# Kernel optimization log

Measured on AMD Instinct MI355X. Metric: run time of the kernel, lower is better.

Reference implementation:

```python
import jax, jax.numpy as jnp
import numpy as np
from jax.scipy import special

B, N, DIM, H, DK, DV, F = 2, 1536, 1536, 8, 64, 64, 192


def _pos_embed(seq_len, feat):
    """Enformer relative positional basis: [2*seq_len-1, feat]."""
    per = feat // 6  # 3 basis families x (symmetric, antisymmetric)
    d = jnp.arange(-seq_len + 1, seq_len, dtype=jnp.float32)
    ad = jnp.abs(d)[:, None]  # [2N-1, 1]
    # exponential decay, log-spaced half lives
    half_life = 2.0 ** jnp.linspace(3.0, float(np.log2(seq_len)), per)
    expo = jnp.exp(-jnp.log(2.0) / half_life * ad)
    # central binary mask
    widths = 2.0 ** jnp.arange(1, per + 1, dtype=jnp.float32) - 1.0
    cmask = (widths > ad).astype(jnp.float32)
    # gamma pdf basis
    stddev = seq_len / (2.0 * per)
    start_mean = seq_len / per
    mean = jnp.linspace(start_mean, float(seq_len), per)
    conc = (mean / stddev) ** 2
    rate = mean / stddev ** 2
    log_unnorm = special.xlogy(conc - 1.0, ad) - rate * ad
    log_norm = special.gammaln(conc) - conc * jnp.log(rate)
    probs = jnp.exp(log_unnorm - log_norm) + 1e-8
    gamma = probs / jnp.max(probs, axis=-1, keepdims=True)
    emb = jnp.concatenate([expo, cmask, gamma], axis=-1)
    emb = jnp.concatenate([emb, jnp.sign(d)[:, None] * emb], axis=-1)
    return emb.astype(jnp.float32)


def _relative_shift(x):
    # x: [B, H, N, 2N-1] -> [B, H, N, N] (Transformer-XL shift)
    b, h, t1, t2 = x.shape
    x = jnp.pad(x, ((0, 0), (0, 0), (0, 0), (1, 0)))  # [B,H,N,2N]
    x = x.reshape(b, h, t2 + 1, t1)[:, :, 1:, :].reshape(b, h, t1, t2)
    return x[..., : (t2 + 2) // 2]


def setup_inputs() -> dict:
    key = jax.random.key(0)
    ks = jax.random.split(key, 8)
    s = 0.02
    return {
        "x": jax.random.normal(ks[0], (B, N, DIM), dtype=jnp.float32),
        "Wq": jax.random.normal(ks[1], (DIM, H * DK), dtype=jnp.float32) * s,
        "Wk": jax.random.normal(ks[2], (DIM, H * DK), dtype=jnp.float32) * s,
        "Wv": jax.random.normal(ks[3], (DIM, H * DV), dtype=jnp.float32) * s,
        "Wrel": jax.random.normal(ks[4], (F, H * DK), dtype=jnp.float32) * s,
        "Wout": jax.random.normal(ks[5], (H * DV, DIM), dtype=jnp.float32) * s,
        "bout": jnp.zeros((DIM,), dtype=jnp.float32),
        "rel_content_bias": jax.random.normal(ks[6], (1, H, 1, DK), dtype=jnp.float32),
        "rel_pos_bias": jax.random.normal(ks[7], (1, H, 1, DK), dtype=jnp.float32),
        "pos_embed": _pos_embed(N, F),  # [2N-1, F] buffer
    }


def reference(x, Wq, Wk, Wv, Wrel, Wout, bout, rel_content_bias, rel_pos_bias, pos_embed):
    b, n, _ = x.shape
    h, dk = rel_content_bias.shape[1], rel_content_bias.shape[3]
    dv = Wv.shape[1] // h
    scale = dk ** -0.5
    q = (x @ Wq).reshape(b, n, h, dk).transpose(0, 2, 1, 3) * scale  # [b,h,n,dk]
    k = (x @ Wk).reshape(b, n, h, dk).transpose(0, 2, 1, 3)
    v = (x @ Wv).reshape(b, n, h, dv).transpose(0, 2, 1, 3)
    content_logits = jnp.einsum('bhid,bhjd->bhij', q + rel_content_bias, k)
    rel_k = (pos_embed @ Wrel).reshape(-1, h, dk).transpose(1, 0, 2)  # [h,2n-1,dk]
    rel_logits = jnp.einsum('bhid,hjd->bhij', q + rel_pos_bias, rel_k)  # [b,h,n,2n-1]
    rel_logits = _relative_shift(rel_logits)  # [b,h,n,n]
    attn = jax.nn.softmax(content_logits + rel_logits, axis=-1)
    out = jnp.einsum('bhij,bhjd->bhid', attn, v)
    out = out.transpose(0, 2, 1, 3).reshape(b, n, h * dv)
    return out @ Wout + bout
```

## Files before the change

### kernel.cpp

```cpp
#include <hip/hip_runtime.h>

#define NSEQ  1536
#define HEADS 8
#define NREL  3071
#define NRELP 3072

typedef __bf16 bf16;
typedef __bf16 bf16x8 __attribute__((ext_vector_type(8)));
typedef __bf16 bf16x4 __attribute__((ext_vector_type(4)));
typedef float  f32x4  __attribute__((ext_vector_type(4)));

static __device__ __forceinline__ f32x4 mfma16(bf16x8 a, bf16x8 b, f32x4 c) {
  return __builtin_amdgcn_mfma_f32_16x16x32_bf16(a, b, c, 0, 0, 0);
}

static __device__ __forceinline__ void gload_lds16(const bf16* g, bf16* l) {
  __builtin_amdgcn_global_load_lds((const __attribute__((address_space(1))) void*)g,
                                   (__attribute__((address_space(3))) void*)l, 16, 0, 0);
}

#define DPP_F(v, ctrl) __int_as_float(__builtin_amdgcn_update_dpp(0, __float_as_int(v), ctrl, 0xF, 0xF, true))
static __device__ __forceinline__ float rowsum16(float v) {
  v += DPP_F(v, 0xB1);
  v += DPP_F(v, 0x4E);
  v += DPP_F(v, 0x124);
  v += DPP_F(v, 0x128);
  return v;
}

__global__ __launch_bounds__(256) void prep(const float* __restrict__ x, const float* __restrict__ pos,
                                            const float* __restrict__ Wq, const float* __restrict__ Wk,
                                            const float* __restrict__ Wv, const float* __restrict__ Wout,
                                            const float* __restrict__ Wrel,
                                            bf16* __restrict__ xb, bf16* __restrict__ posb,
                                            bf16* __restrict__ WT, bf16* __restrict__ WoT,
                                            bf16* __restrict__ WrT) {
  int blk = blockIdx.x;
  if (blk < 4608) {
    int i = blk * 256 + threadIdx.x;
    float4 v = ((const float4*)x)[i];
    bf16x4 o;
    o[0] = (bf16)v.x; o[1] = (bf16)v.y; o[2] = (bf16)v.z; o[3] = (bf16)v.w;
    ((bf16x4*)xb)[i] = o;
    return;
  }
  blk -= 4608;
  if (blk < 576) {
    int i = blk * 256 + threadIdx.x;
    if (i < (NREL * 192 / 4)) {
      float4 v = ((const float4*)pos)[i];
      bf16x4 o;
      o[0] = (bf16)v.x; o[1] = (bf16)v.y; o[2] = (bf16)v.z; o[3] = (bf16)v.w;
      ((bf16x4*)posb)[i] = o;
    }
    return;
  }
  blk -= 576;
  const float* in; bf16* out; int C, ostride, orowoff, cx, ry;
  if (blk < 768)       { in = Wq;   out = WT;  C = 512;  ostride = 1536; orowoff = 0;    cx = blk % 16; ry = blk / 16; }
  else if (blk < 1536) { blk -= 768;  in = Wk;   out = WT;  C = 512;  ostride = 1536; orowoff = 512;  cx = blk % 16; ry = blk / 16; }
  else if (blk < 2304) { blk -= 1536; in = Wv;   out = WT;  C = 512;  ostride = 1536; orowoff = 1024; cx = blk % 16; ry = blk / 16; }
  else if (blk < 3072) { blk -= 2304; in = Wout; out = WoT; C = 1536; ostride = 512;  orowoff = 0;    cx = blk % 48; ry = blk / 48; }
  else                 { blk -= 3072; in = Wrel; out = WrT; C = 512;  ostride = 192;  orowoff = 0;    cx = blk % 16; ry = blk / 16; }
  __shared__ float t[32][33];
  int tx = threadIdx.x & 31, ty = threadIdx.x >> 5;
  int r0 = ry * 32, c0 = cx * 32;
#pragma unroll
  for (int i = 0; i < 4; i++)
    t[ty + 8 * i][tx] = in[(size_t)(r0 + ty + 8 * i) * C + c0 + tx];
  __syncthreads();
#pragma unroll
  for (int i = 0; i < 4; i++)
    out[(size_t)(c0 + ty + 8 * i + orowoff) * ostride + r0 + tx] = (bf16)t[tx][ty + 8 * i];
}

static __device__ __forceinline__ void gemm_core(const bf16* __restrict__ A, const bf16* __restrict__ BT,
                                                 int Klen, int ldk, int m0, int n0, int M,
                                                 bf16* sa, bf16* sb, f32x4 acc[4][2]) {
  int tid = threadIdx.x, wave = tid >> 6, lane = tid & 63;
  int l15 = lane & 15, quad = lane >> 4;
  int lrow = lane >> 3, lcg = lane & 7;
  for (int k0 = 0; k0 < Klen; k0 += 64) {
    __syncthreads();
#pragma unroll
    for (int t = 0; t < 2; t++) {
      int row = wave * 16 + t * 8 + lrow;
      int ra = m0 + row; if (ra > M - 1) ra = M - 1;
      gload_lds16(A + (size_t)ra * ldk + k0 + ((lcg ^ (row & 7)) * 8), sa + (wave * 16 + t * 8) * 64);
    }
#pragma unroll
    for (int t = 0; t < 4; t++) {
      int row = wave * 32 + t * 8 + lrow;
      gload_lds16(BT + (size_t)(n0 + row) * ldk + k0 + ((lcg ^ (row & 7)) * 8), sb + (wave * 32 + t * 8) * 64);
    }
    __syncthreads();
#pragma unroll
    for (int kq = 0; kq < 2; kq++) {
      bf16x8 af[4], bfr[2];
#pragma unroll
      for (int rt = 0; rt < 4; rt++) {
        int row = rt * 16 + l15;
        af[rt] = *(const bf16x8*)&sa[row * 64 + (((kq * 4 + quad) ^ (row & 7)) * 8)];
      }
#pragma unroll
      for (int ct = 0; ct < 2; ct++) {
        int row = wave * 32 + ct * 16 + l15;
        bfr[ct] = *(const bf16x8*)&sb[row * 64 + (((kq * 4 + quad) ^ (row & 7)) * 8)];
      }
#pragma unroll
      for (int ct = 0; ct < 2; ct++)
#pragma unroll
        for (int rt = 0; rt < 4; rt++)
          acc[rt][ct] = mfma16(af[rt], bfr[ct], acc[rt][ct]);
    }
  }
}

__global__ __launch_bounds__(256) void gemm_qkv(const bf16* __restrict__ xb, const bf16* __restrict__ WT,
                                                const float* __restrict__ cb, const float* __restrict__ pb,
                                                bf16* __restrict__ qc, bf16* __restrict__ qp,
                                                bf16* __restrict__ kb, bf16* __restrict__ vt) {
  __shared__ __align__(16) bf16 sa[64 * 64];
  __shared__ __align__(16) bf16 sb[128 * 64];
  __shared__ __align__(16) bf16 tv[64 * 130];
  int tid = threadIdx.x, wave = tid >> 6, lane = tid & 63;
  int l15 = lane & 15, quad = lane >> 4;
  int m0 = blockIdx.x * 64, n0 = blockIdx.y * 128;
  f32x4 acc[4][2] = {};
  gemm_core(xb, WT, 1536, 1536, m0, n0, 3072, sa, sb, acc);
  int b = m0 / NSEQ, nseq0 = m0 % NSEQ;
  if (blockIdx.y < 8) {
    bool isq = blockIdx.y < 4;
#pragma unroll
    for (int rt = 0; rt < 4; rt++)
#pragma unroll
      for (int ct = 0; ct < 2; ct++)
#pragma unroll
        for (int r = 0; r < 4; r++) {
          int row = nseq0 + rt * 16 + quad * 4 + r;
          int colg = n0 + wave * 32 + ct * 16 + l15;
          int col = colg & 511;
          int h = col >> 6, d = col & 63;
          size_t o = ((size_t)(b * 8 + h) * NSEQ + row) * 64 + d;
          float v = acc[rt][ct][r];
          if (isq) {
            float qv = v * 0.18033688011f;
            qc[o] = (bf16)(qv + cb[col] * 1.44269504089f);
            qp[o] = (bf16)(qv + pb[col] * 1.44269504089f);
          } else {
            kb[o] = (bf16)v;
          }
        }
  } else {
#pragma unroll
    for (int rt = 0; rt < 4; rt++)
#pragma unroll
      for (int ct = 0; ct < 2; ct++)
#pragma unroll
        for (int r = 0; r < 4; r++)
          tv[(rt * 16 + quad * 4 + r) * 130 + wave * 32 + ct * 16 + l15] = (bf16)acc[rt][ct][r];
    __syncthreads();
    int n = tid & 63, c0v = tid >> 6;
    int hbase = (blockIdx.y - 8) * 2;
#pragma unroll
    for (int hh = 0; hh < 2; hh++)
#pragma unroll
      for (int i = 0; i < 16; i++) {
        int dv = i * 4 + c0v;
        vt[((size_t)(b * 8 + hbase + hh) * 64 + dv) * NSEQ + nseq0 + n] = tv[n * 130 + hh * 64 + dv];
      }
  }
}

__global__ __launch_bounds__(256) void gemm_rel(const bf16* __restrict__ posb, const bf16* __restrict__ WrT,
                                                bf16* __restrict__ rk) {
  __shared__ __align__(16) bf16 sa[64 * 64];
  __shared__ __align__(16) bf16 sb[128 * 64];
  int tid = threadIdx.x, wave = tid >> 6, lane = tid & 63;
  int l15 = lane & 15, quad = lane >> 4;
  int m0 = blockIdx.x * 64, n0 = blockIdx.y * 128;
  f32x4 acc[4][2] = {};
  gemm_core(posb, WrT, 192, 192, m0, n0, NREL, sa, sb, acc);
#pragma unroll
  for (int rt = 0; rt < 4; rt++)
#pragma unroll
    for (int ct = 0; ct < 2; ct++)
#pragma unroll
      for (int r = 0; r < 4; r++) {
        int row = m0 + rt * 16 + quad * 4 + r;
        if (row < NREL) {
          int col = n0 + wave * 32 + ct * 16 + l15;
          rk[((size_t)(col >> 6) * NRELP + row) * 64 + (col & 63)] = (bf16)acc[rt][ct][r];
        }
      }
}

__global__ __launch_bounds__(256) void gemm_out(const bf16* __restrict__ A, const bf16* __restrict__ BT,
                                                float* __restrict__ C, const float* __restrict__ bias) {
  __shared__ __align__(16) bf16 sa[64 * 64];
  __shared__ __align__(16) bf16 sb[128 * 64];
  int tid = threadIdx.x, wave = tid >> 6, lane = tid & 63;
  int l15 = lane & 15, quad = lane >> 4;
  int m0 = blockIdx.x * 64, n0 = blockIdx.y * 128;
  f32x4 acc[4][2] = {};
  gemm_core(A, BT, 512, 512, m0, n0, 3072, sa, sb, acc);
#pragma unroll
  for (int rt = 0; rt < 4; rt++)
#pragma unroll
    for (int ct = 0; ct < 2; ct++)
#pragma unroll
      for (int r = 0; r < 4; r++) {
        int row = m0 + rt * 16 + quad * 4 + r;
        int col = n0 + wave * 32 + ct * 16 + l15;
        C[(size_t)row * 1536 + col] = acc[rt][ct][r] + bias[col];
      }
}

__global__ __launch_bounds__(256, 4) void attn(const bf16* __restrict__ qc, const bf16* __restrict__ qp,
                                               const bf16* __restrict__ kb, const bf16* __restrict__ vt,
                                               const bf16* __restrict__ rk,
                                               float* __restrict__ Opart, float* __restrict__ mlp) {
  __shared__ __align__(16) bf16 sk[64 * 64];
  __shared__ __align__(16) bf16 sv[64 * 64];
  __shared__ __align__(16) bf16 srel[128 * 64];
  __shared__ __align__(16) bf16 pls[4][16 * 64];
  int qb = blockIdx.x, bh = blockIdx.y, kz = blockIdx.z;
  int h = bh & 7;
  int i0 = qb * 64;
  int wave = threadIdx.x >> 6, lane = threadIdx.x & 63;
  int l15 = lane & 15, quad = lane >> 4;
  int lrow = lane >> 3, lcg = lane & 7;
  const bf16* qcb = qc + (size_t)bh * NSEQ * 64;
  const bf16* qpb = qp + (size_t)bh * NSEQ * 64;
  const bf16* kbb = kb + (size_t)bh * NSEQ * 64;
  const bf16* vtb = vt + (size_t)bh * 64 * NSEQ;
  const bf16* rkh = rk + (size_t)h * NRELP * 64;
  bf16* plsw = pls[wave];

  int qrow = i0 + wave * 16 + l15;
  bf16x8 aqc0 = *(const bf16x8*)(qcb + (size_t)qrow * 64 + quad * 8);
  bf16x8 aqc1 = *(const bf16x8*)(qcb + (size_t)qrow * 64 + 32 + quad * 8);
  bf16x8 aqp0 = *(const bf16x8*)(qpb + (size_t)qrow * 64 + quad * 8);
  bf16x8 aqp1 = *(const bf16x8*)(qpb + (size_t)qrow * 64 + 32 + quad * 8);

  int bidx[4];
  bool hisel[4];
#pragma unroll
  for (int r = 0; r < 4; r++) {
    int rl = quad * 4 + r;
    bidx[r] = (quad * 16 + ((l15 + 15 - rl) & 15)) << 2;
    hisel[r] = l15 > rl;
  }

  int swz = (lcg ^ lrow) * 8;
  int jb = 23 + kz * 12 - qb;
  const bf16* pK = kbb + (size_t)(kz * 768 + wave * 16 + lrow) * 64 + swz;
  const bf16* pV = vtb + (size_t)(wave * 16 + lrow) * NSEQ + kz * 768 + swz;
  const bf16* pR = rkh + (size_t)(jb + 1) * 4096 + (size_t)(wave * 16 + lrow) * 64 + swz;
  bf16* dK = sk + wave * 1024;
  bf16* dV = sv + wave * 1024;

  {
    const bf16* pP = rkh + (size_t)jb * 4096 + (size_t)(wave * 16 + lrow) * 64 + swz;
    bf16* dP = srel + ((jb & 1) * 64 + wave * 16) * 64;
#pragma unroll
    for (int t = 0; t < 2; t++)
      gload_lds16(pP + t * 512, dP + t * 512);
  }
  int pxor = (jb & 1) << 6;

  int swzA = (quad ^ (l15 & 7)) * 8;
  int swzB = ((4 + quad) ^ (l15 & 7)) * 8;
  int rb0 = (3 - wave) * 16 + l15;
  int pxl = (l15 >> 1) << 3;
  const bf16* plr = plsw + l15 * 64;

  f32x4 acco[4] = {};
  float li[4] = {0.0f, 0.0f, 0.0f, 0.0f};

  for (int jt = 0; jt < 12; jt++) {
    __syncthreads();
#pragma unroll
    for (int t = 0; t < 2; t++) gload_lds16(pK + t * 512, dK + t * 512);
#pragma unroll
    for (int t = 0; t < 2; t++) gload_lds16(pV + (size_t)t * 8 * NSEQ, dV + t * 512);
    {
      bf16* dR = srel + (pxor ^ 64) * 64 + wave * 1024;
#pragma unroll
      for (int t = 0; t < 2; t++) gload_lds16(pR + t * 512, dR + t * 512);
    }
    __syncthreads();
    f32x4 s[4] = {};
#pragma unroll
    for (int c = 0; c < 4; c++) {
      const bf16* kp = sk + (c * 16 + l15) * 64;
      s[c] = mfma16(aqc0, *(const bf16x8*)(kp + swzA), s[c]);
      s[c] = mfma16(aqc1, *(const bf16x8*)(kp + swzB), s[c]);
    }
    f32x4 sb5[5];
#pragma unroll
    for (int cc = 0; cc < 5; cc++) {
      const bf16* rp = srel + ((rb0 + cc * 16) ^ pxor) * 64;
      f32x4 z = {};
      z = mfma16(aqp0, *(const bf16x8*)(rp + swzA), z);
      sb5[cc] = mfma16(aqp1, *(const bf16x8*)(rp + swzB), z);
    }
#pragma unroll
    for (int r = 0; r < 4; r++) {
      float bp[5];
#pragma unroll
      for (int cc = 0; cc < 5; cc++)
        bp[cc] = __int_as_float(__builtin_amdgcn_ds_bpermute(bidx[r], __float_as_int(sb5[cc][r])));
#pragma unroll
      for (int c = 0; c < 4; c++)
        s[c][r] += hisel[r] ? bp[c + 1] : bp[c];
    }
#pragma unroll
    for (int c = 0; c < 4; c++)
#pragma unroll
      for (int r = 0; r < 4; r++) {
        float p = __builtin_amdgcn_exp2f(s[c][r] - 11.5415603f);
        bf16 pbh = (bf16)p;
        li[r] += (float)pbh;
        int prow = quad * 4 + r;
        plsw[prow * 64 + ((c * 16 + l15) ^ ((prow >> 1) << 3))] = pbh;
      }
#pragma unroll
    for (int ks = 0; ks < 2; ks++) {
      bf16x8 ap = *(const bf16x8*)(plr + ((ks * 32 + quad * 8) ^ pxl));
#pragma unroll
      for (int c = 0; c < 4; c++) {
        const bf16* vp = sv + (c * 16 + l15) * 64;
        acco[c] = mfma16(ap, *(const bf16x8*)(vp + (ks ? swzB : swzA)), acco[c]);
      }
    }
    pK += 4096; pV += 64; pR += 4096; pxor ^= 64;
  }
#pragma unroll
  for (int r = 0; r < 4; r++)
    li[r] = rowsum16(li[r]);
  int qt16 = qb * 4 + wave;
  size_t pbase = ((size_t)(bh * 96 + qt16) * 2 + kz);
#pragma unroll
  for (int c = 0; c < 4; c++)
#pragma unroll
    for (int r = 0; r < 4; r++)
      Opart[pbase * 1024 + (quad * 4 + r) * 64 + c * 16 + l15] = acco[c][r];
  if (l15 == 0) {
#pragma unroll
    for (int r = 0; r < 4; r++)
      mlp[pbase * 16 + quad * 4 + r] = li[r];
  }
}

__global__ void attn_merge(const float* __restrict__ Opart, const float* __restrict__ mlp,
                           bf16* __restrict__ O) {
  int qt = blockIdx.x, bh = blockIdx.y;
  int b = bh >> 3, h = bh & 7;
  int col = threadIdx.x & 63, rg = threadIdx.x >> 6;
  size_t base = (size_t)(bh * 96 + qt) * 2;
#pragma unroll
  for (int rr = 0; rr < 4; rr++) {
    int row = rg * 4 + rr;
    float L = mlp[base * 16 + row] + mlp[(base + 1) * 16 + row];
    float v = Opart[base * 1024 + row * 64 + col] + Opart[(base + 1) * 1024 + row * 64 + col];
    O[((size_t)(b * NSEQ + qt * 16 + row) * 8 + h) * 64 + col] = (bf16)(v / L);
  }
}

extern "C" void kernel_launch(void* const* d_in, const int* in_sizes, int n_in,
                              void* d_out, int out_size, void* d_ws, size_t ws_size,
                              hipStream_t stream) {
  const float* x    = (const float*)d_in[0];
  const float* Wq   = (const float*)d_in[1];
  const float* Wk   = (const float*)d_in[2];
  const float* Wv   = (const float*)d_in[3];
  const float* Wrel = (const float*)d_in[4];
  const float* Wout = (const float*)d_in[5];
  const float* bout = (const float*)d_in[6];
  const float* cb   = (const float*)d_in[7];
  const float* pb   = (const float*)d_in[8];
  const float* pos  = (const float*)d_in[9];
  float* out = (float*)d_out;

  char* ws = (char*)d_ws;
  size_t off = 0;
  auto alloc = [&](size_t bytes) {
    char* p = ws + off;
    off = (off + bytes + 255) & ~(size_t)255;
    return p;
  };
  bf16*  xb    = (bf16*)alloc(3072UL * 1536 * 2);
  bf16*  WT    = (bf16*)alloc(1536UL * 1536 * 2);
  bf16*  WoT   = (bf16*)alloc(1536UL * 512 * 2);
  bf16*  WrT   = (bf16*)alloc(512UL * 192 * 2);
  bf16*  posb  = (bf16*)alloc((size_t)NREL * 192 * 2);
  bf16*  qcb   = (bf16*)alloc(16UL * NSEQ * 64 * 2);
  bf16*  qpb   = (bf16*)alloc(16UL * NSEQ * 64 * 2);
  bf16*  kbb   = (bf16*)alloc(16UL * NSEQ * 64 * 2);
  bf16*  vtb   = (bf16*)alloc(16UL * NSEQ * 64 * 2);
  bf16*  rkb   = (bf16*)alloc(8UL * NRELP * 64 * 2);
  bf16*  Ob    = (bf16*)alloc(3072UL * 512 * 2);
  float* Opart = (float*)alloc(16UL * 96 * 2 * 1024 * 4);
  float* mlpw  = (float*)alloc(16UL * 96 * 2 * 16 * 4);

  prep<<<dim3(8352), 256, 0, stream>>>(x, pos, Wq, Wk, Wv, Wout, Wrel, xb, posb, WT, WoT, WrT);
  gemm_qkv<<<dim3(48, 12), 256, 0, stream>>>(xb, WT, cb, pb, qcb, qpb, kbb, vtb);
  gemm_rel<<<dim3(48, 4), 256, 0, stream>>>(posb, WrT, rkb);
  attn<<<dim3(24, 16, 2), 256, 0, stream>>>(qcb, qpb, kbb, vtb, rkb, Opart, mlpw);
  attn_merge<<<dim3(96, 16), 256, 0, stream>>>(Opart, mlpw, Ob);
  gemm_out<<<dim3(48, 12), 256, 0, stream>>>(Ob, WoT, out, bout);
}
```

Baseline: 175.1 us.

## Merge QKV and rel GEMMs into one launch; register-prefetch attention K/V/R tiles

Folds the relative-position GEMM into the QKV projection kernel as extra grid columns, removing one launch and letting the two GEMMs share the GPU. In the attention kernel, the per-iteration direct global-to-LDS loads of K, V and rel-K tiles become register prefetches of the next tile, stored to LDS at the start of each iteration. The intent is to overlap global load latency with the MFMA work of the current tile. The cost is extra VGPRs for the staged tiles, which may lower occupancy.

```diff
diff --git a/kernel.cpp b/kernel.cpp
--- a/kernel.cpp
+++ b/kernel.cpp
@@ -116,17 +116,37 @@
   }
 }
 
-__global__ __launch_bounds__(256) void gemm_qkv(const bf16* __restrict__ xb, const bf16* __restrict__ WT,
-                                                const float* __restrict__ cb, const float* __restrict__ pb,
-                                                bf16* __restrict__ qc, bf16* __restrict__ qp,
-                                                bf16* __restrict__ kb, bf16* __restrict__ vt) {
+__global__ __launch_bounds__(256) void gemm_qkvrel(const bf16* __restrict__ xb, const bf16* __restrict__ WT,
+                                                   const bf16* __restrict__ posb, const bf16* __restrict__ WrT,
+                                                   const float* __restrict__ cb, const float* __restrict__ pb,
+                                                   bf16* __restrict__ qc, bf16* __restrict__ qp,
+                                                   bf16* __restrict__ kb, bf16* __restrict__ vt,
+                                                   bf16* __restrict__ rk) {
   __shared__ __align__(16) bf16 sa[64 * 64];
   __shared__ __align__(16) bf16 sb[128 * 64];
   __shared__ __align__(16) bf16 tv[64 * 130];
   int tid = threadIdx.x, wave = tid >> 6, lane = tid & 63;
   int l15 = lane & 15, quad = lane >> 4;
-  int m0 = blockIdx.x * 64, n0 = blockIdx.y * 128;
+  int m0 = blockIdx.x * 64;
   f32x4 acc[4][2] = {};
+  if (blockIdx.y >= 12) {
+    int n0 = (blockIdx.y - 12) * 128;
+    gemm_core(posb, WrT, 192, 192, m0, n0, NREL, sa, sb, acc);
+#pragma unroll
+    for (int rt = 0; rt < 4; rt++)
+#pragma unroll
+      for (int ct = 0; ct < 2; ct++)
+#pragma unroll
+        for (int r = 0; r < 4; r++) {
+          int row = m0 + rt * 16 + quad * 4 + r;
+          if (row < NREL) {
+            int col = n0 + wave * 32 + ct * 16 + l15;
+            rk[((size_t)(col >> 6) * NRELP + row) * 64 + (col & 63)] = (bf16)acc[rt][ct][r];
+          }
+        }
+    return;
+  }
+  int n0 = blockIdx.y * 128;
   gemm_core(xb, WT, 1536, 1536, m0, n0, 3072, sa, sb, acc);
   int b = m0 / NSEQ, nseq0 = m0 % NSEQ;
   if (blockIdx.y < 8) {
@@ -170,29 +190,6 @@
         vt[((size_t)(b * 8 + hbase + hh) * 64 + dv) * NSEQ + nseq0 + n] = tv[n * 130 + hh * 64 + dv];
       }
   }
-}
-
-__global__ __launch_bounds__(256) void gemm_rel(const bf16* __restrict__ posb, const bf16* __restrict__ WrT,
-                                                bf16* __restrict__ rk) {
-  __shared__ __align__(16) bf16 sa[64 * 64];
-  __shared__ __align__(16) bf16 sb[128 * 64];
-  int tid = threadIdx.x, wave = tid >> 6, lane = tid & 63;
-  int l15 = lane & 15, quad = lane >> 4;
-  int m0 = blockIdx.x * 64, n0 = blockIdx.y * 128;
-  f32x4 acc[4][2] = {};
-  gemm_core(posb, WrT, 192, 192, m0, n0, NREL, sa, sb, acc);
-#pragma unroll
-  for (int rt = 0; rt < 4; rt++)
-#pragma unroll
-    for (int ct = 0; ct < 2; ct++)
-#pragma unroll
-      for (int r = 0; r < 4; r++) {
-        int row = m0 + rt * 16 + quad * 4 + r;
-        if (row < NREL) {
-          int col = n0 + wave * 32 + ct * 16 + l15;
-          rk[((size_t)(col >> 6) * NRELP + row) * 64 + (col & 63)] = (bf16)acc[rt][ct][r];
-        }
-      }
 }
 
 __global__ __launch_bounds__(256) void gemm_out(const bf16* __restrict__ A, const bf16* __restrict__ BT,
@@ -257,8 +254,9 @@
   const bf16* pK = kbb + (size_t)(kz * 768 + wave * 16 + lrow) * 64 + swz;
   const bf16* pV = vtb + (size_t)(wave * 16 + lrow) * NSEQ + kz * 768 + swz;
   const bf16* pR = rkh + (size_t)(jb + 1) * 4096 + (size_t)(wave * 16 + lrow) * 64 + swz;
-  bf16* dK = sk + wave * 1024;
-  bf16* dV = sv + wave * 1024;
+  bf16* wK = sk + (wave * 16 + lrow) * 64 + lcg * 8;
+  bf16* wV = sv + (wave * 16 + lrow) * 64 + lcg * 8;
+  int wRoff = (wave * 16 + lrow) * 64 + lcg * 8;
 
   {
     const bf16* pP = rkh + (size_t)jb * 4096 + (size_t)(wave * 16 + lrow) * 64 + swz;
@@ -267,6 +265,9 @@
     for (int t = 0; t < 2; t++)
       gload_lds16(pP + t * 512, dP + t * 512);
   }
+  float4 kr0 = *(const float4*)(pK), kr1 = *(const float4*)(pK + 512);             pK += 4096;
+  float4 vr0 = *(const float4*)(pV), vr1 = *(const float4*)(pV + 8 * NSEQ);        pV += 64;
+  float4 rr0 = *(const float4*)(pR), rr1 = *(const float4*)(pR + 512);             pR += 4096;
   int pxor = (jb & 1) << 6;
 
   int swzA = (quad ^ (l15 & 7)) * 8;
@@ -280,16 +281,18 @@
 
   for (int jt = 0; jt < 12; jt++) {
     __syncthreads();
-#pragma unroll
-    for (int t = 0; t < 2; t++) gload_lds16(pK + t * 512, dK + t * 512);
-#pragma unroll
-    for (int t = 0; t < 2; t++) gload_lds16(pV + (size_t)t * 8 * NSEQ, dV + t * 512);
+    *(float4*)(wK) = kr0;        *(float4*)(wK + 512) = kr1;
+    *(float4*)(wV) = vr0;        *(float4*)(wV + 512) = vr1;
     {
-      bf16* dR = srel + (pxor ^ 64) * 64 + wave * 1024;
-#pragma unroll
-      for (int t = 0; t < 2; t++) gload_lds16(pR + t * 512, dR + t * 512);
+      bf16* wR = srel + (pxor ^ 64) * 64 + wRoff;
+      *(float4*)(wR) = rr0;      *(float4*)(wR + 512) = rr1;
     }
     __syncthreads();
+    if (jt < 11) {
+      kr0 = *(const float4*)(pK); kr1 = *(const float4*)(pK + 512);        pK += 4096;
+      vr0 = *(const float4*)(pV); vr1 = *(const float4*)(pV + 8 * NSEQ);   pV += 64;
+      rr0 = *(const float4*)(pR); rr1 = *(const float4*)(pR + 512);        pR += 4096;
+    }
     f32x4 s[4] = {};
 #pragma unroll
     for (int c = 0; c < 4; c++) {
@@ -334,7 +337,7 @@
         acco[c] = mfma16(ap, *(const bf16x8*)(vp + (ks ? swzB : swzA)), acco[c]);
       }
     }
-    pK += 4096; pV += 64; pR += 4096; pxor ^= 64;
+    pxor ^= 64;
   }
 #pragma unroll
   for (int r = 0; r < 4; r++)
@@ -405,8 +408,7 @@
   float* mlpw  = (float*)alloc(16UL * 96 * 2 * 16 * 4);
 
   prep<<<dim3(8352), 256, 0, stream>>>(x, pos, Wq, Wk, Wv, Wout, Wrel, xb, posb, WT, WoT, WrT);
-  gemm_qkv<<<dim3(48, 12), 256, 0, stream>>>(xb, WT, cb, pb, qcb, qpb, kbb, vtb);
-  gemm_rel<<<dim3(48, 4), 256, 0, stream>>>(posb, WrT, rkb);
+  gemm_qkvrel<<<dim3(48, 16), 256, 0, stream>>>(xb, WT, posb, WrT, cb, pb, qcb, qpb, kbb, vtb, rkb);
   attn<<<dim3(24, 16, 2), 256, 0, stream>>>(qcb, qpb, kbb, vtb, rkb, Opart, mlpw);
   attn_merge<<<dim3(96, 16), 256, 0, stream>>>(Opart, mlpw, Ob);
   gemm_out<<<dim3(48, 12), 256, 0, stream>>>(Ob, WoT, out, bout);
```

Measured after the change: 171.2 us. -2.2%, faster.
